# Kernel tuning notes

Measured on AMD Instinct MI355X. Metric: run time of the kernel, lower is better.

The kernel has to match this reference:

```python
import jax, jax.numpy as jnp
import numpy as np

V = 50257   # vocab_size
D = 768     # d_model
NL = 4      # n_layers
DI = 1536   # d_inner = expand * d_model
DS = 16     # d_state
DC = 4      # d_conv
B = 2       # batch
L = 512     # seq_len
EPS = 1e-5  # RMSNorm eps
STD = 0.02  # init std


def setup_inputs() -> dict:
    key = jax.random.key(0)
    ks = jax.random.split(key, 8)
    idx = jax.random.randint(ks[0], (B, L), 0, V)
    emb = jax.random.normal(ks[1], (V, D), dtype=jnp.float32) * STD          # tied embedding / lm_head
    W_in = jax.random.normal(ks[2], (NL, 2 * DI, D), dtype=jnp.float32) * STD
    conv_w = jax.random.normal(ks[3], (NL, DI, 1, DC), dtype=jnp.float32) * STD  # depthwise conv [O,I/g,K]
    W_xproj = jax.random.normal(ks[4], (NL, 2 * DS + 1, DI), dtype=jnp.float32) * STD
    W_dt = jax.random.normal(ks[5], (NL, DI, 1), dtype=jnp.float32) * STD    # dt_rank = 1
    b_dt = jnp.zeros((NL, DI), dtype=jnp.float32)
    a_log = jnp.tile(jnp.log(jnp.arange(1, DS + 1, dtype=jnp.float32)), (NL, DI, 1))
    d_param = jnp.ones((NL, DI), dtype=jnp.float32)
    W_out = jax.random.normal(ks[6], (NL, D, DI), dtype=jnp.float32) * STD
    norm_w = jnp.ones((D,), dtype=jnp.float32)
    return dict(idx=idx, emb=emb, W_in=W_in, conv_w=conv_w, W_xproj=W_xproj,
                W_dt=W_dt, b_dt=b_dt, a_log=a_log, d_param=d_param,
                W_out=W_out, norm_w=norm_w)


def _mamba_block(x, W_in, conv_w, W_xproj, W_dt, b_dt, a_log, d_param, W_out):
    # in_proj + split into x, z
    xz = jnp.einsum('bld,ed->ble', x, W_in)            # [B,L,2*DI]
    xs, z = jnp.split(xz, 2, axis=-1)
    # causal depthwise conv1d (torch pads d_conv-1 both sides, keeps first L -> left pad only)
    xc = jnp.transpose(xs, (0, 2, 1))                  # [B,DI,L]
    xc = jax.lax.conv_general_dilated(xc, conv_w, window_strides=(1,),
                                      padding=[(DC - 1, 0)],
                                      feature_group_count=DI,
                                      dimension_numbers=('NCH', 'OIH', 'NCH'))
    xs = jax.nn.silu(jnp.transpose(xc, (0, 2, 1)))     # [B,L,DI]
    # selective SSM
    A = -jnp.exp(a_log)                                # [DI,DS]
    xp = jnp.einsum('bld,ed->ble', xs, W_xproj)        # [B,L,2*DS+1]
    dt_raw = xp[..., 0]                                # [B,L]
    Bp = xp[..., 1:1 + DS]                             # [B,L,DS]
    Cp = xp[..., 1 + DS:]                              # [B,L,DS]
    delta = jax.nn.softplus(dt_raw[..., None] * W_dt[:, 0] + b_dt)  # [B,L,DI]

    def step(h, inp):
        d_i, b_i, c_i, x_i = inp                       # [B,DI],[B,DS],[B,DS],[B,DI]
        a_bar = jnp.exp(d_i[:, :, None] * A)           # [B,DI,DS]
        h = a_bar * h + d_i[:, :, None] * b_i[:, None, :] * x_i[:, :, None]
        y = jnp.einsum('bn,bdn->bd', c_i, h) + d_param * x_i
        return h, y

    h0 = jnp.zeros((x.shape[0], DI, DS), dtype=x.dtype)
    seq = (jnp.moveaxis(delta, 1, 0), jnp.moveaxis(Bp, 1, 0),
           jnp.moveaxis(Cp, 1, 0), jnp.moveaxis(xs, 1, 0))
    _, ys = jax.lax.scan(step, h0, seq)
    y = jnp.moveaxis(ys, 0, 1)                         # [B,L,DI]
    y = y * jax.nn.silu(z)
    return jnp.einsum('ble,de->bld', y, W_out)         # [B,L,D]


def reference(idx, emb, W_in, conv_w, W_xproj, W_dt, b_dt, a_log, d_param, W_out, norm_w):
    x = emb[idx]                                       # [B,L,D]

    def layer(carry, p):
        w_in, c_w, w_xp, w_dt, bdt, alog, dpar, w_out = p
        out = carry + _mamba_block(carry, w_in, c_w, w_xp, w_dt, bdt, alog, dpar, w_out)
        return out, None

    x, _ = jax.lax.scan(layer, x, (W_in, conv_w, W_xproj, W_dt, b_dt, a_log, d_param, W_out))
    rms = jax.lax.rsqrt(jnp.mean(x * x, axis=-1, keepdims=True) + EPS)
    x = x * rms * norm_w
    logits = jnp.einsum('bld,vd->blv', x, emb)         # tied lm_head
    return logits
```

## Files before the change

kernel.cpp:

```cpp
#include <hip/hip_runtime.h>
#include <cstdint>

#define VV     50257
#define VPAD   50304
#define DMODEL 768
#define NLAYER 4
#define DINNER 1536
#define DSTATE 16
#define DCONV  4
#define BATCH  2
#define SEQ    512
#define MROWS  (BATCH*SEQ)

typedef unsigned short u16;
typedef __attribute__((ext_vector_type(8))) short bf16x8;
typedef __attribute__((ext_vector_type(4))) float f32x4;

__device__ __forceinline__ u16 f2bf(float f) {
  unsigned u = __float_as_uint(f);
  u += 0x7fffu + ((u >> 16) & 1u);
  return (u16)(u >> 16);
}

__device__ __forceinline__ void async16(const void* g, void* l) {
  auto gp = reinterpret_cast<const __attribute__((address_space(1))) unsigned int*>(
      reinterpret_cast<uintptr_t>(g));
  auto lp = reinterpret_cast<__attribute__((address_space(3))) unsigned int*>(
      reinterpret_cast<uintptr_t>(l));
  __builtin_amdgcn_global_load_lds(gp, lp, 16, 0, 0);
}

__global__ void cvt_kern(const float* __restrict__ src, u16* __restrict__ dst, int n4) {
  int i = blockIdx.x * blockDim.x + threadIdx.x;
  int stride = gridDim.x * blockDim.x;
  for (; i < n4; i += stride) {
    float4 v = *(const float4*)(src + (long)i * 4);
    ushort4 o; o.x = f2bf(v.x); o.y = f2bf(v.y); o.z = f2bf(v.z); o.w = f2bf(v.w);
    *(ushort4*)(dst + (long)i * 4) = o;
  }
}

__global__ void cvt_pad_kern(const float* __restrict__ src, u16* __restrict__ dst,
                             int nsrc4, int ntot4) {
  int i = blockIdx.x * blockDim.x + threadIdx.x;
  int stride = gridDim.x * blockDim.x;
  for (; i < ntot4; i += stride) {
    ushort4 o;
    if (i < nsrc4) {
      float4 v = *(const float4*)(src + (long)i * 4);
      o.x = f2bf(v.x); o.y = f2bf(v.y); o.z = f2bf(v.z); o.w = f2bf(v.w);
    } else {
      o.x = 0; o.y = 0; o.z = 0; o.w = 0;
    }
    *(ushort4*)(dst + (long)i * 4) = o;
  }
}

__global__ void embed_kern(const int* __restrict__ idx, const float* __restrict__ emb,
                           float* __restrict__ x, u16* __restrict__ xbf) {
  int i4 = blockIdx.x * blockDim.x + threadIdx.x;
  if (i4 >= MROWS * (DMODEL / 4)) return;
  int r = i4 / (DMODEL / 4);
  int c = (i4 % (DMODEL / 4)) * 4;
  int id = idx[r];
  float4 v = *(const float4*)(emb + (long)id * DMODEL + c);
  *(float4*)(x + (long)r * DMODEL + c) = v;
  ushort4 o; o.x = f2bf(v.x); o.y = f2bf(v.y); o.z = f2bf(v.z); o.w = f2bf(v.w);
  *(ushort4*)(xbf + (long)r * DMODEL + c) = o;
}

template<bool ADD, bool WBF, bool GUARDN, bool XSWZ>
__global__ __launch_bounds__(256) void gemm_bt_kern(
    const u16* __restrict__ A, const u16* __restrict__ B,
    float* __restrict__ C, u16* __restrict__ Cbf,
    int M, int N, int K, int lda, int ldb)
{
  __shared__ u16 As[128 * 64];
  __shared__ u16 Bs[128 * 64];
  int bx, by;
  if (XSWZ) {
    const int nt = gridDim.x >> 3;
    const int t = (blockIdx.x & 7) * nt + (blockIdx.x >> 3);
    bx = t & 7; by = t >> 3;
  } else { bx = blockIdx.x; by = blockIdx.y; }
  const int koff = blockIdx.z * K;
  const long coff = (long)blockIdx.z * M * N;

  const int tid  = threadIdx.x;
  const int wave = tid >> 6;
  const int lane = tid & 63;
  const int wr = wave >> 1, wc = wave & 1;
  const int m0 = bx * 128;
  const int n0 = by * 128;
  const int lrow = lane >> 3;
  const int lsw  = (lane & 7) ^ lrow;

  f32x4 acc[4][4];
#pragma unroll
  for (int i = 0; i < 4; ++i)
#pragma unroll
    for (int j = 0; j < 4; ++j) acc[i][j] = (f32x4){0.f, 0.f, 0.f, 0.f};

  const int arow = wr * 64 + (lane & 15);
  const int brow = wc * 64 + (lane & 15);

  for (int k0 = 0; k0 < K; k0 += 64) {
#pragma unroll
    for (int j = 0; j < 4; ++j) {
      const int chunk = (wave << 2) + j;
      const int r = (chunk << 3) + lrow;
      async16(A + ((long)(m0 + r) * lda + koff + k0 + lsw * 8), (char*)As + (chunk << 10));
      async16(B + ((long)(n0 + r) * ldb + koff + k0 + lsw * 8), (char*)Bs + (chunk << 10));
    }
    asm volatile("s_waitcnt vmcnt(0)" ::: "memory");
    __syncthreads();

#pragma unroll
    for (int kk = 0; kk < 64; kk += 32) {
      const int qb = (kk >> 3) + (lane >> 4);
      bf16x8 af[4], bfr[4];
#pragma unroll
      for (int i = 0; i < 4; ++i) {
        const int rr = arow + i * 16;
        af[i] = *(const bf16x8*)(As + rr * 64 + ((qb ^ (rr & 7)) << 3));
      }
#pragma unroll
      for (int j = 0; j < 4; ++j) {
        const int rr = brow + j * 16;
        bfr[j] = *(const bf16x8*)(Bs + rr * 64 + ((qb ^ (rr & 7)) << 3));
      }
#pragma unroll
      for (int i = 0; i < 4; ++i)
#pragma unroll
        for (int j = 0; j < 4; ++j)
          acc[i][j] = __builtin_amdgcn_mfma_f32_16x16x32_bf16(af[i], bfr[j], acc[i][j], 0, 0, 0);
    }
    __syncthreads();
  }

  const int rbase = m0 + wr * 64 + ((lane >> 4) << 2);
  const int cbase = n0 + wc * 64 + (lane & 15);
#pragma unroll
  for (int j = 0; j < 4; ++j) {
    const int col = cbase + j * 16;
    if (GUARDN && col >= N) continue;
#pragma unroll
    for (int i = 0; i < 4; ++i) {
#pragma unroll
      for (int r = 0; r < 4; ++r) {
        const int row = rbase + i * 16 + r;
        const long off = coff + (long)row * N + col;
        float v = acc[i][j][r];
        if (ADD) v += C[off];
        C[off] = v;
        if (WBF) Cbf[off] = f2bf(v);
      }
    }
  }
}

__global__ __launch_bounds__(256) void redout_kern(const float* __restrict__ part,
                                                   float* __restrict__ xf,
                                                   u16* __restrict__ xbf) {
  const int i = blockIdx.x * blockDim.x + threadIdx.x;
  if (i >= MROWS * DMODEL / 4) return;
  const int stride4 = MROWS * DMODEL / 4;
  float4 s = ((const float4*)part)[i];
  float4 p1 = ((const float4*)part)[i + stride4];
  float4 p2 = ((const float4*)part)[i + 2 * stride4];
  float4 p3 = ((const float4*)part)[i + 3 * stride4];
  float4 x = ((const float4*)xf)[i];
  s.x += p1.x + p2.x + p3.x + x.x;
  s.y += p1.y + p2.y + p3.y + x.y;
  s.z += p1.z + p2.z + p3.z + x.z;
  s.w += p1.w + p2.w + p3.w + x.w;
  ((float4*)xf)[i] = s;
  ushort4 o; o.x = f2bf(s.x); o.y = f2bf(s.y); o.z = f2bf(s.z); o.w = f2bf(s.w);
  ((ushort4*)xbf)[i] = o;
}

__global__ __launch_bounds__(256) void convxproj_kern(
    const float* __restrict__ xz, const float* __restrict__ cw,
    const float* __restrict__ Wx, const float* __restrict__ wdt,
    const float* __restrict__ bdt,
    float* __restrict__ xs, float* __restrict__ dlt, float* __restrict__ bc)
{
  __shared__ float sx[DINNER];
  __shared__ float sxp[40];
  const int row = blockIdx.x;
  const int t = row & (SEQ - 1);
  const int tid = threadIdx.x;

  for (int c = tid; c < DINNER; c += 256) {
    const float* w = cw + c * DCONV;
    float a = 0.f;
#pragma unroll
    for (int k = 0; k < DCONV; ++k) {
      const int tt = t - (DCONV - 1) + k;
      if (tt >= 0) a += w[k] * xz[(long)(row - (DCONV - 1) + k) * (2 * DINNER) + c];
    }
    const float s = a / (1.f + __expf(-a));
    sx[c] = s;
    xs[(long)row * DINNER + c] = s;
  }
  __syncthreads();

  const int wv = tid >> 6, lane = tid & 63;
  for (int e = wv; e < 2 * DSTATE + 1; e += 4) {
    const float* We = Wx + (long)e * DINNER;
    float p = 0.f;
    for (int d = lane; d < DINNER; d += 64) p += sx[d] * We[d];
#pragma unroll
    for (int off = 32; off; off >>= 1) p += __shfl_xor(p, off, 64);
    if (lane == 0) sxp[e] = p;
  }
  __syncthreads();
  const float dtr = sxp[0];
  for (int d = tid; d < DINNER; d += 256) {
    float v = dtr * wdt[d] + bdt[d];
    float sp = (v > 15.f) ? v : log1pf(__expf(v));
    dlt[(long)row * DINNER + d] = sp;
  }
  if (tid < 2 * DSTATE) bc[(long)row * (2 * DSTATE) + tid] = sxp[1 + tid];
}

__global__ __launch_bounds__(128) void scan_kern(
    const float* __restrict__ dlt, const float* __restrict__ bc,
    const float* __restrict__ xs, const float* __restrict__ xz,
    const float* __restrict__ alog, const float* __restrict__ dpar,
    u16* __restrict__ ybf)
{
  __shared__ float sh_h[16][8][DSTATE];
  __shared__ float sh_s[16][8];
  const int tid = threadIdx.x;
  const int ch = tid & 7, chunk = tid >> 3;
  const int ch_abs = blockIdx.x * 8 + ch;
  const int b = ch_abs / DINNER, d = ch_abs % DINNER;
  float An[DSTATE];
#pragma unroll
  for (int n = 0; n < DSTATE; ++n) An[n] = -__expf(alog[(long)d * DSTATE + n]);
  const int r0 = b * SEQ + chunk * 32;

  float h[DSTATE];
#pragma unroll
  for (int n = 0; n < DSTATE; ++n) h[n] = 0.f;
  float ssum = 0.f;
  for (int s = 0; s < 32; ++s) {
    const int row = r0 + s;
    const float dl = dlt[(long)row * DINNER + d];
    const float xv = xs[(long)row * DINNER + d];
    const float dx = dl * xv;
    const float4* bp = (const float4*)(bc + (long)row * (2 * DSTATE));
    float Bv[DSTATE];
    *(float4*)&Bv[0]  = bp[0]; *(float4*)&Bv[4]  = bp[1];
    *(float4*)&Bv[8]  = bp[2]; *(float4*)&Bv[12] = bp[3];
    ssum += dl;
#pragma unroll
    for (int n = 0; n < DSTATE; ++n) h[n] = __expf(dl * An[n]) * h[n] + dx * Bv[n];
  }
#pragma unroll
  for (int n = 0; n < DSTATE; ++n) sh_h[chunk][ch][n] = h[n];
  sh_s[chunk][ch] = ssum;
  __syncthreads();

  {
    const int n2 = tid & 15, ch2 = tid >> 4;
    const int d2 = (blockIdx.x * 8 + ch2) % DINNER;
    const float A2 = -__expf(alog[(long)d2 * DSTATE + n2]);
    float carry = 0.f;
    for (int c = 0; c < 16; ++c) {
      const float hl = sh_h[c][ch2][n2];
      sh_h[c][ch2][n2] = carry;
      carry = __expf(A2 * sh_s[c][ch2]) * carry + hl;
    }
  }
  __syncthreads();

#pragma unroll
  for (int n = 0; n < DSTATE; ++n) h[n] = sh_h[chunk][ch][n];
  const float dp = dpar[d];
  for (int s = 0; s < 32; ++s) {
    const int row = r0 + s;
    const float dl = dlt[(long)row * DINNER + d];
    const float xv = xs[(long)row * DINNER + d];
    const float dx = dl * xv;
    const float4* bp = (const float4*)(bc + (long)row * (2 * DSTATE));
    float Bv[DSTATE], Cv[DSTATE];
    *(float4*)&Bv[0]  = bp[0]; *(float4*)&Bv[4]  = bp[1];
    *(float4*)&Bv[8]  = bp[2]; *(float4*)&Bv[12] = bp[3];
    *(float4*)&Cv[0]  = bp[4]; *(float4*)&Cv[4]  = bp[5];
    *(float4*)&Cv[8]  = bp[6]; *(float4*)&Cv[12] = bp[7];
    float y = 0.f;
#pragma unroll
    for (int n = 0; n < DSTATE; ++n) {
      const float hn = __expf(dl * An[n]) * h[n] + dx * Bv[n];
      h[n] = hn;
      y += Cv[n] * hn;
    }
    y += dp * xv;
    const float zz = xz[(long)row * (2 * DINNER) + DINNER + d];
    const float o = y * (zz / (1.f + __expf(-zz)));
    ybf[(long)row * DINNER + d] = f2bf(o);
  }
}

__global__ __launch_bounds__(256) void rmsnorm_kern(const float* __restrict__ x,
                                                    const float* __restrict__ nw,
                                                    u16* __restrict__ xnbf) {
  const int row = blockIdx.x, tid = threadIdx.x;
  const float* xr = x + (long)row * DMODEL;
  float p = 0.f;
#pragma unroll
  for (int k = 0; k < 3; ++k) { float v = xr[tid + k * 256]; p += v * v; }
#pragma unroll
  for (int off = 32; off; off >>= 1) p += __shfl_xor(p, off, 64);
  __shared__ float red[4];
  __shared__ float s_rms;
  const int wv = tid >> 6, lane = tid & 63;
  if (lane == 0) red[wv] = p;
  __syncthreads();
  if (tid == 0) {
    float tsum = red[0] + red[1] + red[2] + red[3];
    s_rms = rsqrtf(tsum / (float)DMODEL + 1e-5f);
  }
  __syncthreads();
  const float r = s_rms;
#pragma unroll
  for (int k = 0; k < 3; ++k) {
    const int dd = tid + k * 256;
    xnbf[(long)row * DMODEL + dd] = f2bf(xr[dd] * r * nw[dd]);
  }
}

extern "C" void kernel_launch(void* const* d_in, const int* in_sizes, int n_in,
                              void* d_out, int out_size, void* d_ws, size_t ws_size,
                              hipStream_t stream)
{
  (void)in_sizes; (void)n_in; (void)out_size; (void)ws_size;
  const int*   idx   = (const int*)  d_in[0];
  const float* emb   = (const float*)d_in[1];
  const float* W_in  = (const float*)d_in[2];
  const float* convw = (const float*)d_in[3];
  const float* W_xp  = (const float*)d_in[4];
  const float* W_dt  = (const float*)d_in[5];
  const float* b_dt  = (const float*)d_in[6];
  const float* a_log = (const float*)d_in[7];
  const float* d_par = (const float*)d_in[8];
  const float* W_out = (const float*)d_in[9];
  const float* normw = (const float*)d_in[10];
  float* out = (float*)d_out;

  char* ws = (char*)d_ws;
  size_t off = 0;
  auto alloc = [&](size_t bytes) -> void* {
    void* p = ws + off;
    off += (bytes + 255) & ~(size_t)255;
    return p;
  };
  u16*   embbf  = (u16*)  alloc((size_t)VPAD * DMODEL * 2);
  u16*   winbf  = (u16*)  alloc((size_t)NLAYER * 2 * DINNER * DMODEL * 2);
  u16*   woutbf = (u16*)  alloc((size_t)NLAYER * DMODEL * DINNER * 2);
  float* xf     = (float*)alloc((size_t)MROWS * DMODEL * 4);
  u16*   xbf    = (u16*)  alloc((size_t)MROWS * DMODEL * 2);
  float* xz     = (float*)alloc((size_t)MROWS * 2 * DINNER * 4);
  float* xs     = (float*)alloc((size_t)MROWS * DINNER * 4);
  float* dlt    = (float*)alloc((size_t)MROWS * DINNER * 4);
  float* bc     = (float*)alloc((size_t)MROWS * 2 * DSTATE * 4);
  u16*   ybf    = (u16*)  alloc((size_t)MROWS * DINNER * 2);
  u16*   xnbf   = (u16*)  alloc((size_t)MROWS * DMODEL * 2);
  float* part   = (float*)alloc((size_t)4 * MROWS * DMODEL * 4);

  cvt_pad_kern<<<4096, 256, 0, stream>>>(emb, embbf, VV * DMODEL / 4, VPAD * DMODEL / 4);
  cvt_kern<<<4096, 256, 0, stream>>>(W_in, winbf, NLAYER * 2 * DINNER * DMODEL / 4);
  cvt_kern<<<2048, 256, 0, stream>>>(W_out, woutbf, NLAYER * DMODEL * DINNER / 4);
  embed_kern<<<(MROWS * DMODEL / 4 + 255) / 256, 256, 0, stream>>>(idx, emb, xf, xbf);

  for (int l = 0; l < NLAYER; ++l) {
    gemm_bt_kern<false, false, false, true><<<8 * (2 * DINNER / 128), 256, 0, stream>>>(
        xbf, winbf + (size_t)l * 2 * DINNER * DMODEL, xz, nullptr,
        MROWS, 2 * DINNER, DMODEL, DMODEL, DMODEL);
    convxproj_kern<<<MROWS, 256, 0, stream>>>(
        xz, convw + (size_t)l * DINNER * DCONV,
        W_xp + (size_t)l * (2 * DSTATE + 1) * DINNER,
        W_dt + (size_t)l * DINNER, b_dt + (size_t)l * DINNER, xs, dlt, bc);
    scan_kern<<<BATCH * DINNER / 8, 128, 0, stream>>>(
        dlt, bc, xs, xz, a_log + (size_t)l * DINNER * DSTATE, d_par + (size_t)l * DINNER, ybf);
    gemm_bt_kern<false, false, false, true><<<dim3(8 * (DMODEL / 128), 1, 4), 256, 0, stream>>>(
        ybf, woutbf + (size_t)l * DMODEL * DINNER, part, nullptr,
        MROWS, DMODEL, DINNER / 4, DINNER, DINNER);
    redout_kern<<<MROWS * DMODEL / 4 / 256, 256, 0, stream>>>(part, xf, xbf);
  }
  rmsnorm_kern<<<MROWS, 256, 0, stream>>>(xf, normw, xnbf);
  gemm_bt_kern<false, false, true, true><<<8 * (VPAD / 128), 256, 0, stream>>>(
      xnbf, embbf, out, nullptr, MROWS, VV, DMODEL, DMODEL, DMODEL);
}
```

Baseline: 942.7 us.

## Triple-buffer GEMM K-loop with async LDS loads and merge prep kernels

Rewrites the bf16 MFMA GEMM to use 32-wide K tiles in a 3-slot LDS ring. Loads for tile t+2 are issued before computing tile t, with partial vmcnt waits and raw s_barrier plus setprio around the MFMA block. This is meant to overlap global-to-LDS traffic with matrix math instead of fully draining loads every iteration. Separately, it fuses the three weight-conversion kernels and the embedding gather into a single prep kernel to cut launch overhead. The cost is more barriers per K and tighter reliance on correct vmcnt accounting.

```diff
diff --git a/kernel.cpp b/kernel.cpp
--- a/kernel.cpp
+++ b/kernel.cpp
@@ -30,53 +30,56 @@
   __builtin_amdgcn_global_load_lds(gp, lp, 16, 0, 0);
 }
 
-__global__ void cvt_kern(const float* __restrict__ src, u16* __restrict__ dst, int n4) {
+__global__ void prep_kern(const float* __restrict__ emb, const float* __restrict__ W_in,
+                          const float* __restrict__ W_out, const int* __restrict__ idx,
+                          u16* __restrict__ embbf, u16* __restrict__ winbf,
+                          u16* __restrict__ woutbf, float* __restrict__ xf,
+                          u16* __restrict__ xbf) {
+  const int E4  = VPAD * DMODEL / 4;
+  const int W14 = NLAYER * 2 * DINNER * DMODEL / 4;
+  const int W24 = NLAYER * DMODEL * DINNER / 4;
+  const int X4  = MROWS * DMODEL / 4;
+  const int TOT = E4 + W14 + W24 + X4;
   int i = blockIdx.x * blockDim.x + threadIdx.x;
-  int stride = gridDim.x * blockDim.x;
-  for (; i < n4; i += stride) {
-    float4 v = *(const float4*)(src + (long)i * 4);
-    ushort4 o; o.x = f2bf(v.x); o.y = f2bf(v.y); o.z = f2bf(v.z); o.w = f2bf(v.w);
-    *(ushort4*)(dst + (long)i * 4) = o;
-  }
-}
-
-__global__ void cvt_pad_kern(const float* __restrict__ src, u16* __restrict__ dst,
-                             int nsrc4, int ntot4) {
-  int i = blockIdx.x * blockDim.x + threadIdx.x;
-  int stride = gridDim.x * blockDim.x;
-  for (; i < ntot4; i += stride) {
-    ushort4 o;
-    if (i < nsrc4) {
-      float4 v = *(const float4*)(src + (long)i * 4);
-      o.x = f2bf(v.x); o.y = f2bf(v.y); o.z = f2bf(v.z); o.w = f2bf(v.w);
+  const int stride = gridDim.x * blockDim.x;
+  for (; i < TOT; i += stride) {
+    if (i < E4) {
+      ushort4 o;
+      if (i < VV * DMODEL / 4) {
+        float4 v = *(const float4*)(emb + (long)i * 4);
+        o.x = f2bf(v.x); o.y = f2bf(v.y); o.z = f2bf(v.z); o.w = f2bf(v.w);
+      } else { o.x = 0; o.y = 0; o.z = 0; o.w = 0; }
+      *(ushort4*)(embbf + (long)i * 4) = o;
+    } else if (i < E4 + W14) {
+      const int j = i - E4;
+      float4 v = *(const float4*)(W_in + (long)j * 4);
+      ushort4 o; o.x = f2bf(v.x); o.y = f2bf(v.y); o.z = f2bf(v.z); o.w = f2bf(v.w);
+      *(ushort4*)(winbf + (long)j * 4) = o;
+    } else if (i < E4 + W14 + W24) {
+      const int j = i - E4 - W14;
+      float4 v = *(const float4*)(W_out + (long)j * 4);
+      ushort4 o; o.x = f2bf(v.x); o.y = f2bf(v.y); o.z = f2bf(v.z); o.w = f2bf(v.w);
+      *(ushort4*)(woutbf + (long)j * 4) = o;
     } else {
-      o.x = 0; o.y = 0; o.z = 0; o.w = 0;
-    }
-    *(ushort4*)(dst + (long)i * 4) = o;
-  }
-}
-
-__global__ void embed_kern(const int* __restrict__ idx, const float* __restrict__ emb,
-                           float* __restrict__ x, u16* __restrict__ xbf) {
-  int i4 = blockIdx.x * blockDim.x + threadIdx.x;
-  if (i4 >= MROWS * (DMODEL / 4)) return;
-  int r = i4 / (DMODEL / 4);
-  int c = (i4 % (DMODEL / 4)) * 4;
-  int id = idx[r];
-  float4 v = *(const float4*)(emb + (long)id * DMODEL + c);
-  *(float4*)(x + (long)r * DMODEL + c) = v;
-  ushort4 o; o.x = f2bf(v.x); o.y = f2bf(v.y); o.z = f2bf(v.z); o.w = f2bf(v.w);
-  *(ushort4*)(xbf + (long)r * DMODEL + c) = o;
-}
-
-template<bool ADD, bool WBF, bool GUARDN, bool XSWZ>
-__global__ __launch_bounds__(256) void gemm_bt_kern(
+      const int j = i - E4 - W14 - W24;
+      const int r = j / (DMODEL / 4);
+      const int c = (j % (DMODEL / 4)) * 4;
+      const int id = idx[r];
+      float4 v = *(const float4*)(emb + (long)id * DMODEL + c);
+      *(float4*)(xf + (long)r * DMODEL + c) = v;
+      ushort4 o; o.x = f2bf(v.x); o.y = f2bf(v.y); o.z = f2bf(v.z); o.w = f2bf(v.w);
+      *(ushort4*)(xbf + (long)r * DMODEL + c) = o;
+    }
+  }
+}
+
+template<bool GUARDN, bool XSWZ>
+__global__ __launch_bounds__(256) void gemm3_kern(
     const u16* __restrict__ A, const u16* __restrict__ B,
-    float* __restrict__ C, u16* __restrict__ Cbf,
-    int M, int N, int K, int lda, int ldb)
+    float* __restrict__ C, int M, int N, int K, int lda, int ldb)
 {
-  __shared__ u16 As[128 * 64];
-  __shared__ u16 Bs[128 * 64];
+  __shared__ u16 As[3][128 * 32];
+  __shared__ u16 Bs[3][128 * 32];
   int bx, by;
   if (XSWZ) {
     const int nt = gridDim.x >> 3;
@@ -92,8 +95,9 @@
   const int wr = wave >> 1, wc = wave & 1;
   const int m0 = bx * 128;
   const int n0 = by * 128;
-  const int lrow = lane >> 3;
-  const int lsw  = (lane & 7) ^ lrow;
+
+  const int srow = wave * 32 + (lane >> 2);
+  const int sblk = ((lane & 3) ^ ((lane >> 3) & 3)) * 8;
 
   f32x4 acc[4][4];
 #pragma unroll
@@ -103,39 +107,55 @@
 
   const int arow = wr * 64 + (lane & 15);
   const int brow = wc * 64 + (lane & 15);
-
-  for (int k0 = 0; k0 < K; k0 += 64) {
-#pragma unroll
-    for (int j = 0; j < 4; ++j) {
-      const int chunk = (wave << 2) + j;
-      const int r = (chunk << 3) + lrow;
-      async16(A + ((long)(m0 + r) * lda + koff + k0 + lsw * 8), (char*)As + (chunk << 10));
-      async16(B + ((long)(n0 + r) * ldb + koff + k0 + lsw * 8), (char*)Bs + (chunk << 10));
-    }
-    asm volatile("s_waitcnt vmcnt(0)" ::: "memory");
-    __syncthreads();
-
-#pragma unroll
-    for (int kk = 0; kk < 64; kk += 32) {
-      const int qb = (kk >> 3) + (lane >> 4);
-      bf16x8 af[4], bfr[4];
-#pragma unroll
-      for (int i = 0; i < 4; ++i) {
-        const int rr = arow + i * 16;
-        af[i] = *(const bf16x8*)(As + rr * 64 + ((qb ^ (rr & 7)) << 3));
-      }
-#pragma unroll
-      for (int j = 0; j < 4; ++j) {
-        const int rr = brow + j * 16;
-        bfr[j] = *(const bf16x8*)(Bs + rr * 64 + ((qb ^ (rr & 7)) << 3));
-      }
-#pragma unroll
-      for (int i = 0; i < 4; ++i)
-#pragma unroll
-        for (int j = 0; j < 4; ++j)
-          acc[i][j] = __builtin_amdgcn_mfma_f32_16x16x32_bf16(af[i], bfr[j], acc[i][j], 0, 0, 0);
-    }
-    __syncthreads();
+  const int sa   = (((lane >> 4) ^ ((lane >> 1) & 3)) << 3);
+
+  const int KT = K / 32;
+  auto stage = [&](int kt) {
+    const int slot = kt % 3;
+    const long kcol = (long)koff + kt * 32;
+#pragma unroll
+    for (int j = 0; j < 2; ++j) {
+      async16(A + (long)(m0 + srow + j * 16) * lda + kcol + sblk,
+              (char*)(As[slot]) + (wave * 32 + j * 16) * 64);
+      async16(B + (long)(n0 + srow + j * 16) * ldb + kcol + sblk,
+              (char*)(Bs[slot]) + (wave * 32 + j * 16) * 64);
+    }
+  };
+
+  stage(0);
+  stage(1);
+  for (int t = 0; t < KT; ++t) {
+    if (t + 2 < KT) {
+      stage(t + 2);
+      asm volatile("s_waitcnt vmcnt(8)" ::: "memory");
+    } else if (t + 2 == KT) {
+      asm volatile("s_waitcnt vmcnt(4)" ::: "memory");
+    } else {
+      asm volatile("s_waitcnt vmcnt(0)" ::: "memory");
+    }
+    __builtin_amdgcn_s_barrier();
+    asm volatile("" ::: "memory");
+
+    const int slot = t % 3;
+    const u16* as = As[slot];
+    const u16* bs = Bs[slot];
+    bf16x8 af[4], bv[4];
+#pragma unroll
+    for (int i = 0; i < 4; ++i) af[i] = *(const bf16x8*)(as + (arow + 16 * i) * 32 + sa);
+#pragma unroll
+    for (int j = 0; j < 4; ++j) bv[j] = *(const bf16x8*)(bs + (brow + 16 * j) * 32 + sa);
+
+    __builtin_amdgcn_s_setprio(1);
+#pragma unroll
+    for (int i = 0; i < 4; ++i)
+#pragma unroll
+      for (int j = 0; j < 4; ++j)
+        acc[i][j] = __builtin_amdgcn_mfma_f32_16x16x32_bf16(af[i], bv[j], acc[i][j], 0, 0, 0);
+    __builtin_amdgcn_s_setprio(0);
+
+    asm volatile("" ::: "memory");
+    __builtin_amdgcn_s_barrier();
+    asm volatile("" ::: "memory");
   }
 
   const int rbase = m0 + wr * 64 + ((lane >> 4) << 2);
@@ -149,11 +169,7 @@
 #pragma unroll
       for (int r = 0; r < 4; ++r) {
         const int row = rbase + i * 16 + r;
-        const long off = coff + (long)row * N + col;
-        float v = acc[i][j][r];
-        if (ADD) v += C[off];
-        C[off] = v;
-        if (WBF) Cbf[off] = f2bf(v);
+        C[coff + (long)row * N + col] = acc[i][j][r];
       }
     }
   }
@@ -370,14 +386,11 @@
   u16*   xnbf   = (u16*)  alloc((size_t)MROWS * DMODEL * 2);
   float* part   = (float*)alloc((size_t)4 * MROWS * DMODEL * 4);
 
-  cvt_pad_kern<<<4096, 256, 0, stream>>>(emb, embbf, VV * DMODEL / 4, VPAD * DMODEL / 4);
-  cvt_kern<<<4096, 256, 0, stream>>>(W_in, winbf, NLAYER * 2 * DINNER * DMODEL / 4);
-  cvt_kern<<<2048, 256, 0, stream>>>(W_out, woutbf, NLAYER * DMODEL * DINNER / 4);
-  embed_kern<<<(MROWS * DMODEL / 4 + 255) / 256, 256, 0, stream>>>(idx, emb, xf, xbf);
+  prep_kern<<<2048, 256, 0, stream>>>(emb, W_in, W_out, idx, embbf, winbf, woutbf, xf, xbf);
 
   for (int l = 0; l < NLAYER; ++l) {
-    gemm_bt_kern<false, false, false, true><<<8 * (2 * DINNER / 128), 256, 0, stream>>>(
-        xbf, winbf + (size_t)l * 2 * DINNER * DMODEL, xz, nullptr,
+    gemm3_kern<false, true><<<8 * (2 * DINNER / 128), 256, 0, stream>>>(
+        xbf, winbf + (size_t)l * 2 * DINNER * DMODEL, xz,
         MROWS, 2 * DINNER, DMODEL, DMODEL, DMODEL);
     convxproj_kern<<<MROWS, 256, 0, stream>>>(
         xz, convw + (size_t)l * DINNER * DCONV,
@@ -385,12 +398,12 @@
         W_dt + (size_t)l * DINNER, b_dt + (size_t)l * DINNER, xs, dlt, bc);
     scan_kern<<<BATCH * DINNER / 8, 128, 0, stream>>>(
         dlt, bc, xs, xz, a_log + (size_t)l * DINNER * DSTATE, d_par + (size_t)l * DINNER, ybf);
-    gemm_bt_kern<false, false, false, true><<<dim3(8 * (DMODEL / 128), 1, 4), 256, 0, stream>>>(
-        ybf, woutbf + (size_t)l * DMODEL * DINNER, part, nullptr,
+    gemm3_kern<false, true><<<dim3(8 * (DMODEL / 128), 1, 4), 256, 0, stream>>>(
+        ybf, woutbf + (size_t)l * DMODEL * DINNER, part,
         MROWS, DMODEL, DINNER / 4, DINNER, DINNER);
     redout_kern<<<MROWS * DMODEL / 4 / 256, 256, 0, stream>>>(part, xf, xbf);
   }
   rmsnorm_kern<<<MROWS, 256, 0, stream>>>(xf, normw, xnbf);
-  gemm_bt_kern<false, false, true, true><<<8 * (VPAD / 128), 256, 0, stream>>>(
-      xnbf, embbf, out, nullptr, MROWS, VV, DMODEL, DMODEL, DMODEL);
-}
+  gemm3_kern<true, true><<<8 * (VPAD / 128), 256, 0, stream>>>(
+      xnbf, embbf, out, MROWS, VV, DMODEL, DMODEL, DMODEL);
+}
```

Result: faster. 918.8 us (-2.5%).
